# Kernel optimization log

Measured on AMD Instinct MI355X. Metric: run time of the kernel, lower is better.

## Reference

```python
import jax, jax.numpy as jnp
import numpy as np

NOPEN = 64
NNIN = 16
NUM_OUTPUT = 64
NLAYER = 4
H = 0.1
TF = 1.0
N_NODES = 50000
N_EDGES = 1600000


def setup_inputs() -> dict:
    key = jax.random.key(0)
    k1, k2, k3, k4, k5, k6 = jax.random.split(key, 6)
    xn = jax.random.normal(k1, (1, NNIN, N_NODES), dtype=jnp.float32)
    iInd = jax.random.randint(k2, (N_EDGES,), 0, N_NODES)
    jInd = jax.random.randint(k3, (N_EDGES,), 0, N_NODES)
    # learned parameters per original init
    K1Nopen = jax.random.normal(k4, (NOPEN, NNIN), dtype=jnp.float32) * 0.01
    KN1 = jnp.eye(NOPEN, dtype=jnp.float32) + jax.random.uniform(k5, (NOPEN, NOPEN), dtype=jnp.float32) * 0.001
    KNclose = jax.random.normal(k6, (NUM_OUTPUT, NOPEN), dtype=jnp.float32) * 0.01
    return {"xn": xn, "iInd": iInd, "jInd": jInd, "n_nodes": N_NODES,
            "K1Nopen": K1Nopen, "KN1": KN1, "KNclose": KNclose}


def _gcn_norm(I, J, n_nodes, dtype):
    # add self-loops, symmetric normalization deg^{-1/2}[row]*deg^{-1/2}[col]
    loops = jnp.arange(n_nodes, dtype=I.dtype)
    I2 = jnp.concatenate([I, loops])
    J2 = jnp.concatenate([J, loops])
    ew = jnp.ones(I2.shape[0], dtype=dtype)
    deg = jax.ops.segment_sum(ew, J2, num_segments=n_nodes)
    dinv = jnp.where(deg > 0, 1.0 / jnp.sqrt(deg), 0.0)
    w = dinv[I2] * dinv[J2]
    return I2, J2, w


def reference(xn, iInd, jInd, n_nodes, K1Nopen, KN1, KNclose):
    I, J, w = _gcn_norm(iInd, jInd, n_nodes, xn.dtype)  # [E+N]

    # OpenFlatLayer: 1x1 conv1d with K1Nopen + relu (openclose=True, norm=False)
    x = jax.nn.relu(jnp.einsum('oi,bin->bon', K1Nopen, xn))  # [1, nopen, N]

    dt = TF / NLAYER
    wb = w[None, None, :]
    for _ in range(NLAYER):
        # nodeGrad: edge features [1, nopen, E]
        g = wb * (x[:, :, I] - x[:, :, J])
        # singleLayer (openclose=False): conv(K), relu, conv(K.t())
        z = jax.nn.relu(jnp.einsum('oi,bie->boe', KN1, g))
        z = jnp.einsum('io,bie->boe', KN1, z)
        # edgeDiv: scatter-add w*z at I minus at J
        wz = jnp.moveaxis(wb * z, -1, 0)  # [E, 1, nopen]
        div = (jax.ops.segment_sum(wz, I, num_segments=n_nodes)
               - jax.ops.segment_sum(wz, J, num_segments=n_nodes))
        div = jnp.moveaxis(div, 0, -1)  # [1, nopen, N]
        # forward Euler: step layer returns -h*div, integrated with dt
        x = x - dt * H * div

    # CloseLayer: 1x1 conv1d, squeeze().t(), log_softmax over channels
    xc = jnp.einsum('oi,bin->bon', KNclose, x)[0].T  # [N, num_output]
    return jax.nn.log_softmax(xc, axis=1)
```

## Files before the change

kernel.cpp:

```cpp
#include <hip/hip_runtime.h>

#define NN 50000
#define NE 1600000
#define C 64
#define NIN 16
#define DTH 0.025f
#define ASC 16.0f
#define USC 64.0f
#define SDIV 16384.0f
#define SLOT 128

#define NB2 256
#define NPB 196
#define CAP 16384
#define ABLK 1024
#define EPB 1563
#define RND 2048
#define BINC 32
#define GSTR 16

typedef _Float16 f16x2 __attribute__((ext_vector_type(2)));
typedef float f32x2 __attribute__((ext_vector_type(2)));
union U32H2 { uint32_t u; f16x2 h; };

#define RL(x, l) __int_as_float(__builtin_amdgcn_readlane(__float_as_int(x), (l)))

__global__ void k_setup(const float* __restrict__ KN1, const float* __restrict__ KNc,
                        float* __restrict__ M2s, float* __restrict__ KMs,
                        int* __restrict__ gcur) {
    if (threadIdx.x < NB2) gcur[threadIdx.x * GSTR] = 0;
    for (int idx = threadIdx.x; idx < C * C; idx += blockDim.x) {
        int p = idx >> 6, o = idx & 63;
        float s1 = 0.f, s2 = 0.f;
        for (int i = 0; i < C; i++) {
            s1 = fmaf(KN1[o * C + i], KN1[p * C + i], s1);
            s2 = fmaf(KNc[o * C + i], KN1[p * C + i], s2);
        }
        M2s[idx] = s1;
        KMs[idx] = s2;
    }
}

static __device__ __forceinline__ void store_u8(uint32_t* __restrict__ u8, int n, int lane, float su) {
    float v1 = __shfl_down(su, 1, 64);
    float v2 = __shfl_down(su, 2, 64);
    float v3 = __shfl_down(su, 3, 64);
    if ((lane & 3) == 0) {
        int p0 = __builtin_amdgcn_cvt_pk_fp8_f32(su, v1, 0, false);
        int p1 = __builtin_amdgcn_cvt_pk_fp8_f32(v2, v3, p0, true);
        u8[n * 16 + (lane >> 2)] = (uint32_t)p1;
    }
}

__launch_bounds__(512)
__global__ void k_binA_open(const int* __restrict__ iInd, const int* __restrict__ jInd,
                            int* __restrict__ gcur, uint32_t* __restrict__ stg,
                            const float* __restrict__ xn, const float* __restrict__ K1,
                            const float* __restrict__ KN1, const float* __restrict__ KNc,
                            _Float16* __restrict__ u0, uint32_t* __restrict__ u8,
                            float* __restrict__ co) {
    __shared__ __align__(16) char smem[36864];
    __shared__ int bcnt[NB2];
    __shared__ int gbase[NB2];
    uint32_t (*bins)[BINC] = (uint32_t(*)[BINC])smem;
    int tid = threadIdx.x;
    int eBeg = blockIdx.x * EPB;
    int eEnd = eBeg + EPB; if (eEnd > NE) eEnd = NE;
    for (int rb = eBeg; rb < eEnd; rb += RND) {
        for (int b = tid; b < NB2; b += 512) bcnt[b] = 0;
        __syncthreads();
        int rEnd = rb + RND; if (rEnd > eEnd) rEnd = eEnd;
        for (int e = rb + tid; e < rEnd; e += 512) {
            int i = __builtin_nontemporal_load(&iInd[e]);
            int j = __builtin_nontemporal_load(&jInd[e]);
            {
                int b = (unsigned)i / NPB;
                uint32_t ent = ((unsigned)(i - b * NPB) << 17) | (unsigned)j;
                int pos = atomicAdd(&bcnt[b], 1);
                if (pos < BINC) bins[b][pos] = ent;
                else { int gp = atomicAdd(&gcur[b * GSTR], 1);
                       if (gp < CAP) stg[(size_t)b * CAP + gp] = ent; }
            }
            {
                int b = (unsigned)j / NPB;
                uint32_t ent = ((unsigned)(j - b * NPB) << 17) | 0x10000u | (unsigned)i;
                int pos = atomicAdd(&bcnt[b], 1);
                if (pos < BINC) bins[b][pos] = ent;
                else { int gp = atomicAdd(&gcur[b * GSTR], 1);
                       if (gp < CAP) stg[(size_t)b * CAP + gp] = ent; }
            }
        }
        __syncthreads();
        if (tid < NB2) {
            int c = bcnt[tid]; if (c > BINC) c = BINC;
            gbase[tid] = (c > 0) ? atomicAdd(&gcur[tid * GSTR], c) : 0;
        }
        __syncthreads();
        for (int idx = tid; idx < NB2 * BINC; idx += 512) {
            int b = idx >> 5, k = idx & (BINC - 1);
            int c = bcnt[b]; if (c > BINC) c = BINC;
            if (k < c) {
                int pos = gbase[b] + k;
                if (pos < CAP) stg[(size_t)b * CAP + pos] = bins[b][k];
            }
        }
        __syncthreads();
    }
    float* sK1 = (float*)smem;
    float* sU  = sK1 + NIN * C;
    float* sC  = sU + C * C;
    for (int idx = tid; idx < NIN * C; idx += 512) {
        int i = idx >> 6, o = idx & 63;
        sK1[idx] = K1[o * NIN + i];
    }
    for (int idx = tid; idx < C * C; idx += 512) {
        int o = idx >> 6, p = idx & 63;
        int sw = (o << 6) | (p ^ ((o & 7) << 2));
        sU[sw] = KN1[idx];
        sC[sw] = KNc[idx];
    }
    __syncthreads();
    int wv = tid >> 6, lane = tid & 63;
    int mb = lane << 6, lx = (lane & 7) << 2;
    for (int pr = blockIdx.x * 8 + wv; pr < NN / 2; pr += ABLK * 8) {
        int nA = pr * 2, nB = nA + 1;
        float xA = 0.f, xB = 0.f;
#pragma unroll
        for (int i = 0; i < NIN; i++) {
            float k1 = sK1[i * C + lane];
            xA = fmaf(k1, xn[i * NN + nA], xA);
            xB = fmaf(k1, xn[i * NN + nB], xB);
        }
        xA = fmaxf(xA, 0.f); xB = fmaxf(xB, 0.f);
        float uA0 = 0.f, uA1 = 0.f, uB0 = 0.f, uB1 = 0.f;
        float cA0 = 0.f, cA1 = 0.f, cB0 = 0.f, cB1 = 0.f;
#pragma unroll
        for (int p0 = 0; p0 < C; p0 += 4) {
            const float4 mu = *(const float4*)&sU[mb + (p0 ^ lx)];
            const float4 mc = *(const float4*)&sC[mb + (p0 ^ lx)];
            float a0 = RL(xA, p0 + 0), a1 = RL(xA, p0 + 1);
            float a2 = RL(xA, p0 + 2), a3 = RL(xA, p0 + 3);
            float b0 = RL(xB, p0 + 0), b1 = RL(xB, p0 + 1);
            float b2 = RL(xB, p0 + 2), b3 = RL(xB, p0 + 3);
            uA0 = fmaf(mu.x, a0, uA0); uA1 = fmaf(mu.y, a1, uA1);
            uA0 = fmaf(mu.z, a2, uA0); uA1 = fmaf(mu.w, a3, uA1);
            uB0 = fmaf(mu.x, b0, uB0); uB1 = fmaf(mu.y, b1, uB1);
            uB0 = fmaf(mu.z, b2, uB0); uB1 = fmaf(mu.w, b3, uB1);
            cA0 = fmaf(mc.x, a0, cA0); cA1 = fmaf(mc.y, a1, cA1);
            cA0 = fmaf(mc.z, a2, cA0); cA1 = fmaf(mc.w, a3, cA1);
            cB0 = fmaf(mc.x, b0, cB0); cB1 = fmaf(mc.y, b1, cB1);
            cB0 = fmaf(mc.z, b2, cB0); cB1 = fmaf(mc.w, b3, cB1);
        }
        float uA = uA0 + uA1, uB = uB0 + uB1;
        u0[(size_t)nA * C + lane] = (_Float16)uA;
        u0[(size_t)nB * C + lane] = (_Float16)uB;
        store_u8(u8, nA, lane, uA * USC);
        store_u8(u8, nB, lane, uB * USC);
        co[(size_t)nA * C + lane] = cA0 + cA1;
        co[(size_t)nB * C + lane] = cB0 + cB1;
    }
}

#define LADJ (NPB * SLOT)
__launch_bounds__(1024)
__global__ void k_binB(const int* __restrict__ gcur, const uint32_t* __restrict__ stg,
                       unsigned* __restrict__ pk, float* __restrict__ dinv,
                       uint32_t* __restrict__ adjp) {
    __shared__ unsigned lcnt[NPB];
    __shared__ uint32_t ladj[LADJ];
    int b = blockIdx.x, tid = threadIdx.x;
    if (tid < NPB) lcnt[tid] = 0;
    __syncthreads();
    int cnt = gcur[b * GSTR]; if (cnt > CAP) cnt = CAP;
    int n0 = b * NPB;
    for (int k = tid; k < cnt; k += 1024) {
        uint32_t ent = stg[(size_t)b * CAP + k];
        int tl = (int)(ent >> 17);
        unsigned sign = (ent >> 16) & 1u;
        unsigned other = ent & 0xFFFFu;
        unsigned ret = atomicAdd(&lcnt[tl], 1u + (sign << 16));
        unsigned slot = ret & 0xFFFFu;
        if (slot < SLOT) ladj[(tl << 7) + slot] = other | (sign << 31);
    }
    __syncthreads();
    if (tid < NPB) {
        int n = n0 + tid;
        if (n < NN) {
            unsigned v = lcnt[tid];
            unsigned c = v & 0xFFFFu; if (c > SLOT) c = SLOT;
            unsigned deg = (v >> 16) + 1u;
            pk[n] = (deg << 16) | c;
            dinv[n] = 1.0f / sqrtf((float)deg);
        }
    }
    int nval = NN - n0; if (nval > NPB) nval = NPB; if (nval < 0) nval = 0;
    int totv = (nval << 7) >> 2;
    uint4* gdst = (uint4*)(adjp + ((size_t)n0 << 7));
    const uint4* lsrc = (const uint4*)ladj;
    for (int v = tid; v < totv; v += 1024) gdst[v] = lsrc[v];
}

__global__ void k_weight(const unsigned* __restrict__ pk, const float* __restrict__ dinv,
                         uint32_t* __restrict__ adjp) {
    int idx = blockIdx.x * 256 + threadIdx.x;
    int n = idx >> 7, p = idx & (SLOT - 1);
    int cnt = (int)(pk[n] & 0xFFFFu); if (cnt > SLOT) cnt = SLOT;
    int pad = (cnt + 31) & ~31;
    if (p < cnt) {
        uint32_t e = adjp[idx];
        int other = (int)(e & 0xFFFFu);
        float a = ASC * dinv[n] * dinv[other];
        float w = 0.5f * a * a;
        if (e >> 31) w = -w;
        U32H2 t; t.u = (unsigned)other; t.h.y = (_Float16)w;
        adjp[idx] = t.u;
    } else if (p < pad) {
        adjp[idx] = 0u;
    }
}

#define ACCR(WW, QQ, A0, A1, A2, A3, U0, U1, U2, U3) {                        \
    U32H2 aw; aw.u = (WW);                                                    \
    float w_ = (float)aw.h.y;                                                 \
    f32x2 lo_ = __builtin_amdgcn_cvt_pk_f32_fp8((int)(QQ), false);            \
    f32x2 hi_ = __builtin_amdgcn_cvt_pk_f32_fp8((int)(QQ), true);             \
    float d0_ = (U0) - lo_.x, d1_ = (U1) - lo_.y;                             \
    float d2_ = (U2) - hi_.x, d3_ = (U3) - hi_.y;                             \
    A0 = fmaf(w_, __builtin_fabsf(d0_), fmaf(__builtin_fabsf(w_), d0_, A0));  \
    A1 = fmaf(w_, __builtin_fabsf(d1_), fmaf(__builtin_fabsf(w_), d1_, A1));  \
    A2 = fmaf(w_, __builtin_fabsf(d2_), fmaf(__builtin_fabsf(w_), d2_, A2));  \
    A3 = fmaf(w_, __builtin_fabsf(d3_), fmaf(__builtin_fabsf(w_), d3_, A3));  \
}

#define GATHER2_BODY(PKA, ADJP, U8R)                                          \
    uint32_t unqA = (U8R)[nA * 16 + li];                                      \
    uint32_t unqB = (U8R)[nB * 16 + li];                                      \
    f32x2 alo = __builtin_amdgcn_cvt_pk_f32_fp8((int)unqA, false);            \
    f32x2 ahi = __builtin_amdgcn_cvt_pk_f32_fp8((int)unqA, true);             \
    f32x2 blo = __builtin_amdgcn_cvt_pk_f32_fp8((int)unqB, false);            \
    f32x2 bhi = __builtin_amdgcn_cvt_pk_f32_fp8((int)unqB, true);             \
    float uA0 = alo.x, uA1 = alo.y, uA2 = ahi.x, uA3 = ahi.y;                 \
    float uB0 = blo.x, uB1 = blo.y, uB2 = bhi.x, uB3 = bhi.y;                 \
    uint2 pk2_ = *(const uint2*)&(PKA)[nA];                                   \
    int degA = (int)(pk2_.x & 0xFFFFu); if (degA > SLOT) degA = SLOT;         \
    int degB = (int)(pk2_.y & 0xFFFFu); if (degB > SLOT) degB = SLOT;         \
    int padA = (degA + 31) & ~31, padB = (degB + 31) & ~31;                   \
    int baseA = nA << 7, baseB = nB << 7;                                     \
    int maxPad = padA > padB ? padA : padB;                                   \
    float aA0 = 0.f, aA1 = 0.f, aA2 = 0.f, aA3 = 0.f;                         \
    float aB0 = 0.f, aB1 = 0.f, aB2 = 0.f, aB3 = 0.f;                         \
    for (int c0 = 0; c0 < maxPad; c0 += 32) {                                 \
        uint32_t wA[8], qA[8], wB[8], qB[8];                                  \
        bool dA = c0 < padA, dB = c0 < padB;                                  \
        if (dA) {                                                             \
            _Pragma("unroll")                                                 \
            for (int r = 0; r < 8; r++) wA[r] = (ADJP)[baseA + c0 + r * 4 + g]; \
        }                                                                     \
        if (dB) {                                                             \
            _Pragma("unroll")                                                 \
            for (int r = 0; r < 8; r++) wB[r] = (ADJP)[baseB + c0 + r * 4 + g]; \
        }                                                                     \
        if (dA) {                                                             \
            _Pragma("unroll")                                                 \
            for (int r = 0; r < 8; r++) qA[r] = (U8R)[(wA[r] & 0xFFFFu) * 16 + li]; \
        }                                                                     \
        if (dB) {                                                             \
            _Pragma("unroll")                                                 \
            for (int r = 0; r < 8; r++) qB[r] = (U8R)[(wB[r] & 0xFFFFu) * 16 + li]; \
        }                                                                     \
        if (dA) {                                                             \
            _Pragma("unroll")                                                 \
            for (int r = 0; r < 8; r++) ACCR(wA[r], qA[r], aA0, aA1, aA2, aA3, uA0, uA1, uA2, uA3) \
        }                                                                     \
        if (dB) {                                                             \
            _Pragma("unroll")                                                 \
            for (int r = 0; r < 8; r++) ACCR(wB[r], qB[r], aB0, aB1, aB2, aB3, uB0, uB1, uB2, uB3) \
        }                                                                     \
    }                                                                         \
    aA0 += __shfl_xor(aA0, 16, 64); aA0 += __shfl_xor(aA0, 32, 64);           \
    aA1 += __shfl_xor(aA1, 16, 64); aA1 += __shfl_xor(aA1, 32, 64);           \
    aA2 += __shfl_xor(aA2, 16, 64); aA2 += __shfl_xor(aA2, 32, 64);           \
    aA3 += __shfl_xor(aA3, 16, 64); aA3 += __shfl_xor(aA3, 32, 64);           \
    aB0 += __shfl_xor(aB0, 16, 64); aB0 += __shfl_xor(aB0, 32, 64);           \
    aB1 += __shfl_xor(aB1, 16, 64); aB1 += __shfl_xor(aB1, 32, 64);           \
    aB2 += __shfl_xor(aB2, 16, 64); aB2 += __shfl_xor(aB2, 32, 64);           \
    aB3 += __shfl_xor(aB3, 16, 64); aB3 += __shfl_xor(aB3, 32, 64);           \
    float rA0 = __shfl(aA0, lane >> 2, 64), rA1 = __shfl(aA1, lane >> 2, 64); \
    float rA2 = __shfl(aA2, lane >> 2, 64), rA3 = __shfl(aA3, lane >> 2, 64); \
    float rB0 = __shfl(aB0, lane >> 2, 64), rB1 = __shfl(aB1, lane >> 2, 64); \
    float rB2 = __shfl(aB2, lane >> 2, 64), rB3 = __shfl(aB3, lane >> 2, 64); \
    float sA_lane = (lane & 2) ? ((lane & 1) ? rA3 : rA2)                     \
                               : ((lane & 1) ? rA1 : rA0);                    \
    float sB_lane = (lane & 2) ? ((lane & 1) ? rB3 : rB2)                     \
                               : ((lane & 1) ? rB1 : rB0);

#define STAGE_MT(SMT, SRC) {                                                  \
    for (int idx = threadIdx.x; idx < C * C; idx += 256) {                    \
        int p_ = idx >> 6, c_ = idx & 63;                                     \
        (SMT)[(c_ << 6) | (p_ ^ ((c_ & 7) << 2))] = (SRC)[idx];               \
    }                                                                         \
}

#define MATVEC2(SMT, SAV, SBV, DUA, DUB) {                                    \
    float mA0_ = 0.f, mA1_ = 0.f, mB0_ = 0.f, mB1_ = 0.f;                     \
    int mb_ = (lane << 6), lx_ = (lane & 7) << 2;                             \
    _Pragma("unroll")                                                         \
    for (int p0 = 0; p0 < 64; p0 += 4) {                                      \
        const float4 mv = *(const float4*)&(SMT)[mb_ + (p0 ^ lx_)];           \
        mA0_ = fmaf(mv.x, RL(SAV, p0 + 0), mA0_);                             \
        mA1_ = fmaf(mv.y, RL(SAV, p0 + 1), mA1_);                             \
        mA0_ = fmaf(mv.z, RL(SAV, p0 + 2), mA0_);                             \
        mA1_ = fmaf(mv.w, RL(SAV, p0 + 3), mA1_);                             \
        mB0_ = fmaf(mv.x, RL(SBV, p0 + 0), mB0_);                             \
        mB1_ = fmaf(mv.y, RL(SBV, p0 + 1), mB1_);                             \
        mB0_ = fmaf(mv.z, RL(SBV, p0 + 2), mB0_);                             \
        mB1_ = fmaf(mv.w, RL(SBV, p0 + 3), mB1_);                             \
    }                                                                         \
    DUA = mA0_ + mA1_; DUB = mB0_ + mB1_;                                     \
}

__launch_bounds__(256, 8)
__global__ void k_gather_upd(const unsigned* __restrict__ pk, const uint32_t* __restrict__ adjp,
                             const uint32_t* __restrict__ u8r, const _Float16* __restrict__ ucur,
                             const float* __restrict__ M2s, float* __restrict__ sacc,
                             _Float16* __restrict__ unext, uint32_t* __restrict__ u8w, int beta) {
    __shared__ float sMt[C * C];
    STAGE_MT(sMt, M2s)
    __syncthreads();
    int wv = threadIdx.x >> 6, lane = threadIdx.x & 63;
    int g = lane >> 4, li = lane & 15;
    int nA = (blockIdx.x * 4 + wv) * 2;
    int nB = nA + 1;
    GATHER2_BODY(pk, adjp, u8r)
    float duA, duB;
    MATVEC2(sMt, sA_lane, sB_lane, duA, duB)
    float unewA = (float)ucur[(size_t)nA * C + lane] - (DTH / SDIV) * duA;
    float unewB = (float)ucur[(size_t)nB * C + lane] - (DTH / SDIV) * duB;
    unext[(size_t)nA * C + lane] = (_Float16)unewA;
    unext[(size_t)nB * C + lane] = (_Float16)unewB;
    store_u8(u8w, nA, lane, unewA * USC);
    store_u8(u8w, nB, lane, unewB * USC);
    size_t ixA = (size_t)nA * C + lane, ixB = (size_t)nB * C + lane;
    sacc[ixA] = beta ? (sacc[ixA] + sA_lane) : sA_lane;
    sacc[ixB] = beta ? (sacc[ixB] + sB_lane) : sB_lane;
}

__launch_bounds__(256, 8)
__global__ void k_gather_close(const unsigned* __restrict__ pk, const uint32_t* __restrict__ adjp,
                               const uint32_t* __restrict__ u8r, const float* __restrict__ KMs,
                               const float* __restrict__ sacc, const float* __restrict__ co,
                               float* __restrict__ out) {
    __shared__ float sKMt[C * C];
    STAGE_MT(sKMt, KMs)
    __syncthreads();
    int wv = threadIdx.x >> 6, lane = threadIdx.x & 63;
    int g = lane >> 4, li = lane & 15;
    int nA = (blockIdx.x * 4 + wv) * 2;
    int nB = nA + 1;
    GATHER2_BODY(pk, adjp, u8r)
    float stotA = sA_lane + sacc[(size_t)nA * C + lane];
    float stotB = sB_lane + sacc[(size_t)nB * C + lane];
    float dxA, dxB;
    MATVEC2(sKMt, stotA, stotB, dxA, dxB)
    float oA = co[(size_t)nA * C + lane] - (DTH / SDIV) * dxA;
    float oB = co[(size_t)nB * C + lane] - (DTH / SDIV) * dxB;
    float mA = oA, mB = oB;
#pragma unroll
    for (int off2 = 32; off2; off2 >>= 1) {
        mA = fmaxf(mA, __shfl_xor(mA, off2, 64));
        mB = fmaxf(mB, __shfl_xor(mB, off2, 64));
    }
    float sumA = expf(oA - mA), sumB = expf(oB - mB);
#pragma unroll
    for (int off2 = 32; off2; off2 >>= 1) {
        sumA += __shfl_xor(sumA, off2, 64);
        sumB += __shfl_xor(sumB, off2, 64);
    }
    out[(size_t)nA * C + lane] = oA - mA - logf(sumA);
    out[(size_t)nB * C + lane] = oB - mB - logf(sumB);
}

extern "C" void kernel_launch(void* const* d_in, const int* in_sizes, int n_in,
                              void* d_out, int out_size, void* d_ws, size_t ws_size,
                              hipStream_t stream) {
    (void)in_sizes; (void)n_in; (void)out_size; (void)ws_size;
    const float* xn   = (const float*)d_in[0];
    const int* iInd   = (const int*)d_in[1];
    const int* jInd   = (const int*)d_in[2];
    const float* K1   = (const float*)d_in[4];
    const float* KN1  = (const float*)d_in[5];
    const float* KNc  = (const float*)d_in[6];
    float* out = (float*)d_out;

    char* base = (char*)d_ws;
    size_t off = 0;
    auto alloc = [&](size_t bytes) { char* p = base + off; off = (off + bytes + 255) & ~(size_t)255; return p; };
    float* M2s  = (float*)alloc(C * C * 4);
    float* KMs  = (float*)alloc(C * C * 4);
    int* gcur   = (int*)alloc(NB2 * GSTR * 4);
    unsigned* pk = (unsigned*)alloc(NN * 4);
    float* dinv = (float*)alloc(NN * 4);
    float* co   = (float*)alloc((size_t)NN * C * 4);
    float* sacc = (float*)alloc((size_t)NN * C * 4);
    _Float16* ua = (_Float16*)alloc((size_t)NN * C * 2);
    _Float16* ub = (_Float16*)alloc((size_t)NN * C * 2);
    uint32_t* u8a = (uint32_t*)alloc((size_t)NN * 16 * 4);
    uint32_t* u8b = (uint32_t*)alloc((size_t)NN * 16 * 4);
    uint32_t* stg = (uint32_t*)alloc((size_t)NB2 * CAP * 4);
    uint32_t* adjp = (uint32_t*)alloc((size_t)NN * SLOT * 4);

    k_setup<<<1, 256, 0, stream>>>(KN1, KNc, M2s, KMs, gcur);
    k_binA_open<<<ABLK, 512, 0, stream>>>(iInd, jInd, gcur, stg, xn, K1, KN1, KNc, ua, u8a, co);
    k_binB<<<NB2, 1024, 0, stream>>>(gcur, stg, pk, dinv, adjp);
    k_weight<<<(NN * SLOT) / 256, 256, 0, stream>>>(pk, dinv, adjp);

    const int GB = NN / 8;
    k_gather_upd<<<GB, 256, 0, stream>>>(pk, adjp, u8a, ua, M2s, sacc, ub, u8b, 0);
    k_gather_upd<<<GB, 256, 0, stream>>>(pk, adjp, u8b, ub, M2s, sacc, ua, u8a, 1);
    k_gather_upd<<<GB, 256, 0, stream>>>(pk, adjp, u8a, ua, M2s, sacc, ub, u8b, 1);
    k_gather_close<<<GB, 256, 0, stream>>>(pk, adjp, u8b, KMs, sacc, co, out);
}
```

Baseline: 503.3 us.

## Compact padded adjacency into variable-length rows with global offset allocation

Replaces the fixed 128-slot-per-node adjacency with a compacted layout. Each row is padded only to a multiple of 32, and each bin block gets a contiguous region from a global atomic allocator. Bin construction now makes two passes over the staged entries (count, prefix-sum, place), and a per-node row offset array is read by the weight and gather kernels. The aim is to shrink the adjacency footprint and the bytes written, zeroed and copied, so gathers have better cache locality. The cost is an extra staging pass and a serial prefix scan in one thread per block.

```diff
diff --git a/kernel.cpp b/kernel.cpp
--- a/kernel.cpp
+++ b/kernel.cpp
@@ -18,6 +18,7 @@
 #define RND 2048
 #define BINC 32
 #define GSTR 16
+#define LIMG 20480
 
 typedef _Float16 f16x2 __attribute__((ext_vector_type(2)));
 typedef float f32x2 __attribute__((ext_vector_type(2)));
@@ -27,8 +28,9 @@
 
 __global__ void k_setup(const float* __restrict__ KN1, const float* __restrict__ KNc,
                         float* __restrict__ M2s, float* __restrict__ KMs,
-                        int* __restrict__ gcur) {
+                        int* __restrict__ gcur, unsigned* __restrict__ galloc) {
     if (threadIdx.x < NB2) gcur[threadIdx.x * GSTR] = 0;
+    if (threadIdx.x == 0) galloc[0] = 0;
     for (int idx = threadIdx.x; idx < C * C; idx += blockDim.x) {
         int p = idx >> 6, o = idx & 63;
         float s1 = 0.f, s2 = 0.f;
@@ -161,15 +163,18 @@
     }
 }
 
-#define LADJ (NPB * SLOT)
 __launch_bounds__(1024)
 __global__ void k_binB(const int* __restrict__ gcur, const uint32_t* __restrict__ stg,
                        unsigned* __restrict__ pk, float* __restrict__ dinv,
-                       uint32_t* __restrict__ adjp) {
+                       unsigned* __restrict__ rowoff, uint32_t* __restrict__ adjp,
+                       unsigned* __restrict__ galloc) {
     __shared__ unsigned lcnt[NPB];
-    __shared__ uint32_t ladj[LADJ];
+    __shared__ unsigned soff[NPB];
+    __shared__ unsigned place[NPB];
+    __shared__ uint32_t ladj[LIMG];
+    __shared__ unsigned sb[2];
     int b = blockIdx.x, tid = threadIdx.x;
-    if (tid < NPB) lcnt[tid] = 0;
+    if (tid < NPB) { lcnt[tid] = 0; place[tid] = 0; }
     __syncthreads();
     int cnt = gcur[b * GSTR]; if (cnt > CAP) cnt = CAP;
     int n0 = b * NPB;
@@ -177,10 +182,37 @@
         uint32_t ent = stg[(size_t)b * CAP + k];
         int tl = (int)(ent >> 17);
         unsigned sign = (ent >> 16) & 1u;
+        atomicAdd(&lcnt[tl], 1u + (sign << 16));
+    }
+    __syncthreads();
+    if (tid == 0) {
+        unsigned run = 0;
+        for (int t = 0; t < NPB; t++) {
+            unsigned c = lcnt[t] & 0xFFFFu; if (c > SLOT) c = SLOT;
+            soff[t] = run;
+            run += (c + 31u) & ~31u;
+        }
+        sb[1] = run;
+        sb[0] = atomicAdd(galloc, run);
+    }
+    __syncthreads();
+    unsigned bbase = sb[0], total = sb[1];
+    unsigned totl = total < LIMG ? total : LIMG;
+    for (unsigned k = tid; k < totl; k += 1024) ladj[k] = 0u;
+    for (unsigned k = LIMG + tid; k < total; k += 1024) adjp[bbase + k] = 0u;
+    __syncthreads();
+    for (int k = tid; k < cnt; k += 1024) {
+        uint32_t ent = stg[(size_t)b * CAP + k];
+        int tl = (int)(ent >> 17);
+        unsigned sign = (ent >> 16) & 1u;
         unsigned other = ent & 0xFFFFu;
-        unsigned ret = atomicAdd(&lcnt[tl], 1u + (sign << 16));
-        unsigned slot = ret & 0xFFFFu;
-        if (slot < SLOT) ladj[(tl << 7) + slot] = other | (sign << 31);
+        unsigned slot = atomicAdd(&place[tl], 1u);
+        if (slot < SLOT) {
+            unsigned pos = soff[tl] + slot;
+            uint32_t val = other | (sign << 31);
+            if (pos < LIMG) ladj[pos] = val;
+            else adjp[bbase + pos] = val;
+        }
     }
     __syncthreads();
     if (tid < NPB) {
@@ -191,31 +223,29 @@
             unsigned deg = (v >> 16) + 1u;
             pk[n] = (deg << 16) | c;
             dinv[n] = 1.0f / sqrtf((float)deg);
-        }
-    }
-    int nval = NN - n0; if (nval > NPB) nval = NPB; if (nval < 0) nval = 0;
-    int totv = (nval << 7) >> 2;
-    uint4* gdst = (uint4*)(adjp + ((size_t)n0 << 7));
+            rowoff[n] = bbase + soff[tid];
+        }
+    }
+    uint4* gdst = (uint4*)(adjp + bbase);
     const uint4* lsrc = (const uint4*)ladj;
-    for (int v = tid; v < totv; v += 1024) gdst[v] = lsrc[v];
-}
-
-__global__ void k_weight(const unsigned* __restrict__ pk, const float* __restrict__ dinv,
-                         uint32_t* __restrict__ adjp) {
-    int idx = blockIdx.x * 256 + threadIdx.x;
-    int n = idx >> 7, p = idx & (SLOT - 1);
+    for (unsigned v = tid; v < (totl >> 2); v += 1024) gdst[v] = lsrc[v];
+}
+
+__launch_bounds__(256)
+__global__ void k_weight(const unsigned* __restrict__ pk, const unsigned* __restrict__ rowoff,
+                         const float* __restrict__ dinv, uint32_t* __restrict__ adjp) {
+    int n = blockIdx.x * 2 + (threadIdx.x >> 7);
+    int p = threadIdx.x & (SLOT - 1);
     int cnt = (int)(pk[n] & 0xFFFFu); if (cnt > SLOT) cnt = SLOT;
-    int pad = (cnt + 31) & ~31;
     if (p < cnt) {
-        uint32_t e = adjp[idx];
+        unsigned base = rowoff[n];
+        uint32_t e = adjp[base + p];
         int other = (int)(e & 0xFFFFu);
         float a = ASC * dinv[n] * dinv[other];
         float w = 0.5f * a * a;
         if (e >> 31) w = -w;
         U32H2 t; t.u = (unsigned)other; t.h.y = (_Float16)w;
-        adjp[idx] = t.u;
-    } else if (p < pad) {
-        adjp[idx] = 0u;
+        adjp[base + p] = t.u;
     }
 }
 
@@ -232,7 +262,7 @@
     A3 = fmaf(w_, __builtin_fabsf(d3_), fmaf(__builtin_fabsf(w_), d3_, A3));  \
 }
 
-#define GATHER2_BODY(PKA, ADJP, U8R)                                          \
+#define GATHER2_BODY(PKA, ROFF, ADJP, U8R)                                    \
     uint32_t unqA = (U8R)[nA * 16 + li];                                      \
     uint32_t unqB = (U8R)[nB * 16 + li];                                      \
     f32x2 alo = __builtin_amdgcn_cvt_pk_f32_fp8((int)unqA, false);            \
@@ -242,10 +272,11 @@
     float uA0 = alo.x, uA1 = alo.y, uA2 = ahi.x, uA3 = ahi.y;                 \
     float uB0 = blo.x, uB1 = blo.y, uB2 = bhi.x, uB3 = bhi.y;                 \
     uint2 pk2_ = *(const uint2*)&(PKA)[nA];                                   \
+    uint2 ro2_ = *(const uint2*)&(ROFF)[nA];                                  \
     int degA = (int)(pk2_.x & 0xFFFFu); if (degA > SLOT) degA = SLOT;         \
     int degB = (int)(pk2_.y & 0xFFFFu); if (degB > SLOT) degB = SLOT;         \
     int padA = (degA + 31) & ~31, padB = (degB + 31) & ~31;                   \
-    int baseA = nA << 7, baseB = nB << 7;                                     \
+    int baseA = (int)ro2_.x, baseB = (int)ro2_.y;                             \
     int maxPad = padA > padB ? padA : padB;                                   \
     float aA0 = 0.f, aA1 = 0.f, aA2 = 0.f, aA3 = 0.f;                         \
     float aB0 = 0.f, aB1 = 0.f, aB2 = 0.f, aB3 = 0.f;                         \
@@ -320,7 +351,8 @@
 }
 
 __launch_bounds__(256, 8)
-__global__ void k_gather_upd(const unsigned* __restrict__ pk, const uint32_t* __restrict__ adjp,
+__global__ void k_gather_upd(const unsigned* __restrict__ pk, const unsigned* __restrict__ rowoff,
+                             const uint32_t* __restrict__ adjp,
                              const uint32_t* __restrict__ u8r, const _Float16* __restrict__ ucur,
                              const float* __restrict__ M2s, float* __restrict__ sacc,
                              _Float16* __restrict__ unext, uint32_t* __restrict__ u8w, int beta) {
@@ -331,7 +363,7 @@
     int g = lane >> 4, li = lane & 15;
     int nA = (blockIdx.x * 4 + wv) * 2;
     int nB = nA + 1;
-    GATHER2_BODY(pk, adjp, u8r)
+    GATHER2_BODY(pk, rowoff, adjp, u8r)
     float duA, duB;
     MATVEC2(sMt, sA_lane, sB_lane, duA, duB)
     float unewA = (float)ucur[(size_t)nA * C + lane] - (DTH / SDIV) * duA;
@@ -346,7 +378,8 @@
 }
 
 __launch_bounds__(256, 8)
-__global__ void k_gather_close(const unsigned* __restrict__ pk, const uint32_t* __restrict__ adjp,
+__global__ void k_gather_close(const unsigned* __restrict__ pk, const unsigned* __restrict__ rowoff,
+                               const uint32_t* __restrict__ adjp,
                                const uint32_t* __restrict__ u8r, const float* __restrict__ KMs,
                                const float* __restrict__ sacc, const float* __restrict__ co,
                                float* __restrict__ out) {
@@ -357,7 +390,7 @@
     int g = lane >> 4, li = lane & 15;
     int nA = (blockIdx.x * 4 + wv) * 2;
     int nB = nA + 1;
-    GATHER2_BODY(pk, adjp, u8r)
+    GATHER2_BODY(pk, rowoff, adjp, u8r)
     float stotA = sA_lane + sacc[(size_t)nA * C + lane];
     float stotB = sB_lane + sacc[(size_t)nB * C + lane];
     float dxA, dxB;
@@ -398,7 +431,9 @@
     float* M2s  = (float*)alloc(C * C * 4);
     float* KMs  = (float*)alloc(C * C * 4);
     int* gcur   = (int*)alloc(NB2 * GSTR * 4);
+    unsigned* galloc = (unsigned*)alloc(256);
     unsigned* pk = (unsigned*)alloc(NN * 4);
+    unsigned* rowoff = (unsigned*)alloc((NN + 2) * 4);
     float* dinv = (float*)alloc(NN * 4);
     float* co   = (float*)alloc((size_t)NN * C * 4);
     float* sacc = (float*)alloc((size_t)NN * C * 4);
@@ -409,14 +444,14 @@
     uint32_t* stg = (uint32_t*)alloc((size_t)NB2 * CAP * 4);
     uint32_t* adjp = (uint32_t*)alloc((size_t)NN * SLOT * 4);
 
-    k_setup<<<1, 256, 0, stream>>>(KN1, KNc, M2s, KMs, gcur);
+    k_setup<<<1, 256, 0, stream>>>(KN1, KNc, M2s, KMs, gcur, galloc);
     k_binA_open<<<ABLK, 512, 0, stream>>>(iInd, jInd, gcur, stg, xn, K1, KN1, KNc, ua, u8a, co);
-    k_binB<<<NB2, 1024, 0, stream>>>(gcur, stg, pk, dinv, adjp);
-    k_weight<<<(NN * SLOT) / 256, 256, 0, stream>>>(pk, dinv, adjp);
+    k_binB<<<NB2, 1024, 0, stream>>>(gcur, stg, pk, dinv, rowoff, adjp, galloc);
+    k_weight<<<NN / 2, 256, 0, stream>>>(pk, rowoff, dinv, adjp);
 
     const int GB = NN / 8;
-    k_gather_upd<<<GB, 256, 0, stream>>>(pk, adjp, u8a, ua, M2s, sacc, ub, u8b, 0);
-    k_gather_upd<<<GB, 256, 0, stream>>>(pk, adjp, u8b, ub, M2s, sacc, ua, u8a, 1);
-    k_gather_upd<<<GB, 256, 0, stream>>>(pk, adjp, u8a, ua, M2s, sacc, ub, u8b, 1);
-    k_gather_close<<<GB, 256, 0, stream>>>(pk, adjp, u8b, KMs, sacc, co, out);
-}
+    k_gather_upd<<<GB, 256, 0, stream>>>(pk, rowoff, adjp, u8a, ua, M2s, sacc, ub, u8b, 0);
+    k_gather_upd<<<GB, 256, 0, stream>>>(pk, rowoff, adjp, u8b, ub, M2s, sacc, ua, u8a, 1);
+    k_gather_upd<<<GB, 256, 0, stream>>>(pk, rowoff, adjp, u8a, ua, M2s, sacc, ub, u8b, 1);
+    k_gather_close<<<GB, 256, 0, stream>>>(pk, rowoff, adjp, u8b, KMs, sacc, co, out);
+}
```

New measurement: 510.3 us. Within noise of the previous version (+1.4%).

## Fuse edge weight computation into first gather pass and drop k_weight kernel

Applied to the files above, without the earlier changes.

Removes the separate k_weight kernel that rewrote the whole padded adjacency with fp16 edge weights. The first gather layer now loads dinv for each neighbour, computes the signed normalized weight inline, uses it directly, and writes it back into the adjacency for later layers. k_binB now zero-fills the local adjacency so padding entries are already zero. This saves one kernel launch and a full pass over the adjacency buffer, at the cost of an extra dinv gather and predicated stores in the first layer.

```diff
diff --git a/kernel.cpp b/kernel.cpp
--- a/kernel.cpp
+++ b/kernel.cpp
@@ -170,6 +170,7 @@
     __shared__ uint32_t ladj[LADJ];
     int b = blockIdx.x, tid = threadIdx.x;
     if (tid < NPB) lcnt[tid] = 0;
+    for (int k = tid; k < LADJ; k += 1024) ladj[k] = 0u;
     __syncthreads();
     int cnt = gcur[b * GSTR]; if (cnt > CAP) cnt = CAP;
     int n0 = b * NPB;
@@ -200,39 +201,18 @@
     for (int v = tid; v < totv; v += 1024) gdst[v] = lsrc[v];
 }
 
-__global__ void k_weight(const unsigned* __restrict__ pk, const float* __restrict__ dinv,
-                         uint32_t* __restrict__ adjp) {
-    int idx = blockIdx.x * 256 + threadIdx.x;
-    int n = idx >> 7, p = idx & (SLOT - 1);
-    int cnt = (int)(pk[n] & 0xFFFFu); if (cnt > SLOT) cnt = SLOT;
-    int pad = (cnt + 31) & ~31;
-    if (p < cnt) {
-        uint32_t e = adjp[idx];
-        int other = (int)(e & 0xFFFFu);
-        float a = ASC * dinv[n] * dinv[other];
-        float w = 0.5f * a * a;
-        if (e >> 31) w = -w;
-        U32H2 t; t.u = (unsigned)other; t.h.y = (_Float16)w;
-        adjp[idx] = t.u;
-    } else if (p < pad) {
-        adjp[idx] = 0u;
-    }
-}
-
-#define ACCR(WW, QQ, A0, A1, A2, A3, U0, U1, U2, U3) {                        \
-    U32H2 aw; aw.u = (WW);                                                    \
-    float w_ = (float)aw.h.y;                                                 \
+#define ACCR_W(W_, QQ, A0, A1, A2, A3, U0, U1, U2, U3) {                      \
     f32x2 lo_ = __builtin_amdgcn_cvt_pk_f32_fp8((int)(QQ), false);            \
     f32x2 hi_ = __builtin_amdgcn_cvt_pk_f32_fp8((int)(QQ), true);             \
     float d0_ = (U0) - lo_.x, d1_ = (U1) - lo_.y;                             \
     float d2_ = (U2) - hi_.x, d3_ = (U3) - hi_.y;                             \
-    A0 = fmaf(w_, __builtin_fabsf(d0_), fmaf(__builtin_fabsf(w_), d0_, A0));  \
-    A1 = fmaf(w_, __builtin_fabsf(d1_), fmaf(__builtin_fabsf(w_), d1_, A1));  \
-    A2 = fmaf(w_, __builtin_fabsf(d2_), fmaf(__builtin_fabsf(w_), d2_, A2));  \
-    A3 = fmaf(w_, __builtin_fabsf(d3_), fmaf(__builtin_fabsf(w_), d3_, A3));  \
-}
-
-#define GATHER2_BODY(PKA, ADJP, U8R)                                          \
+    A0 = fmaf((W_), __builtin_fabsf(d0_), fmaf(__builtin_fabsf(W_), d0_, A0)); \
+    A1 = fmaf((W_), __builtin_fabsf(d1_), fmaf(__builtin_fabsf(W_), d1_, A1)); \
+    A2 = fmaf((W_), __builtin_fabsf(d2_), fmaf(__builtin_fabsf(W_), d2_, A2)); \
+    A3 = fmaf((W_), __builtin_fabsf(d3_), fmaf(__builtin_fabsf(W_), d3_, A3)); \
+}
+
+#define GATHER2_BODY(PKA, ADJP, U8R, FIRSTF, DINV)                            \
     uint32_t unqA = (U8R)[nA * 16 + li];                                      \
     uint32_t unqB = (U8R)[nB * 16 + li];                                      \
     f32x2 alo = __builtin_amdgcn_cvt_pk_f32_fp8((int)unqA, false);            \
@@ -247,10 +227,13 @@
     int padA = (degA + 31) & ~31, padB = (degB + 31) & ~31;                   \
     int baseA = nA << 7, baseB = nB << 7;                                     \
     int maxPad = padA > padB ? padA : padB;                                   \
+    float dnA = 0.f, dnB = 0.f;                                               \
+    if (FIRSTF) { dnA = ASC * (DINV)[nA]; dnB = ASC * (DINV)[nB]; }           \
     float aA0 = 0.f, aA1 = 0.f, aA2 = 0.f, aA3 = 0.f;                         \
     float aB0 = 0.f, aB1 = 0.f, aB2 = 0.f, aB3 = 0.f;                         \
     for (int c0 = 0; c0 < maxPad; c0 += 32) {                                 \
         uint32_t wA[8], qA[8], wB[8], qB[8];                                  \
+        float vA[8], vB[8];                                                   \
         bool dA = c0 < padA, dB = c0 < padB;                                  \
         if (dA) {                                                             \
             _Pragma("unroll")                                                 \
@@ -260,6 +243,16 @@
             _Pragma("unroll")                                                 \
             for (int r = 0; r < 8; r++) wB[r] = (ADJP)[baseB + c0 + r * 4 + g]; \
         }                                                                     \
+        if (FIRSTF) {                                                         \
+            if (dA) {                                                         \
+                _Pragma("unroll")                                             \
+                for (int r = 0; r < 8; r++) vA[r] = (DINV)[wA[r] & 0xFFFFu];  \
+            }                                                                 \
+            if (dB) {                                                         \
+                _Pragma("unroll")                                             \
+                for (int r = 0; r < 8; r++) vB[r] = (DINV)[wB[r] & 0xFFFFu];  \
+            }                                                                 \
+        }                                                                     \
         if (dA) {                                                             \
             _Pragma("unroll")                                                 \
             for (int r = 0; r < 8; r++) qA[r] = (U8R)[(wA[r] & 0xFFFFu) * 16 + li]; \
@@ -270,11 +263,39 @@
         }                                                                     \
         if (dA) {                                                             \
             _Pragma("unroll")                                                 \
-            for (int r = 0; r < 8; r++) ACCR(wA[r], qA[r], aA0, aA1, aA2, aA3, uA0, uA1, uA2, uA3) \
+            for (int r = 0; r < 8; r++) {                                     \
+                float wgt_;                                                   \
+                if (FIRSTF) {                                                 \
+                    float a_ = dnA * vA[r];                                   \
+                    float wf_ = 0.5f * a_ * a_;                               \
+                    wf_ = __int_as_float(__float_as_int(wf_) ^ (int)(wA[r] & 0x80000000u)); \
+                    if ((c0 + r * 4 + g) >= degA) wf_ = 0.f;                  \
+                    U32H2 t_; t_.u = wA[r] & 0xFFFFu; t_.h.y = (_Float16)wf_; \
+                    wgt_ = (float)t_.h.y;     \
+                    if (li == 2 * r) ((uint32_t*)(ADJP))[baseA + c0 + r * 4 + g] = t_.u; \
+                } else {                                                      \
+                    U32H2 aw_; aw_.u = wA[r]; wgt_ = (float)aw_.h.y;          \
+                }                                                             \
+                ACCR_W(wgt_, qA[r], aA0, aA1, aA2, aA3, uA0, uA1, uA2, uA3)   \
+            }                                                                 \
         }                                                                     \
         if (dB) {                                                             \
             _Pragma("unroll")                                                 \
-            for (int r = 0; r < 8; r++) ACCR(wB[r], qB[r], aB0, aB1, aB2, aB3, uB0, uB1, uB2, uB3) \
+            for (int r = 0; r < 8; r++) {                                     \
+                float wgt_;                                                   \
+                if (FIRSTF) {                                                 \
+                    float a_ = dnB * vB[r];                                   \
+                    float wf_ = 0.5f * a_ * a_;                               \
+                    wf_ = __int_as_float(__float_as_int(wf_) ^ (int)(wB[r] & 0x80000000u)); \
+                    if ((c0 + r * 4 + g) >= degB) wf_ = 0.f;                  \
+                    U32H2 t_; t_.u = wB[r] & 0xFFFFu; t_.h.y = (_Float16)wf_; \
+                    wgt_ = (float)t_.h.y;                                     \
+                    if (li == 2 * r) ((uint32_t*)(ADJP))[baseB + c0 + r * 4 + g] = t_.u; \
+                } else {                                                      \
+                    U32H2 aw_; aw_.u = wB[r]; wgt_ = (float)aw_.h.y;          \
+                }                                                             \
+                ACCR_W(wgt_, qB[r], aB0, aB1, aB2, aB3, uB0, uB1, uB2, uB3)   \
+            }                                                                 \
         }                                                                     \
     }                                                                         \
     aA0 += __shfl_xor(aA0, 16, 64); aA0 += __shfl_xor(aA0, 32, 64);           \
@@ -319,11 +340,13 @@
     DUA = mA0_ + mA1_; DUB = mB0_ + mB1_;                                     \
 }
 
+template<int FIRST>
 __launch_bounds__(256, 8)
-__global__ void k_gather_upd(const unsigned* __restrict__ pk, const uint32_t* __restrict__ adjp,
+__global__ void k_gather_upd(const unsigned* __restrict__ pk, uint32_t* __restrict__ adjp,
                              const uint32_t* __restrict__ u8r, const _Float16* __restrict__ ucur,
                              const float* __restrict__ M2s, float* __restrict__ sacc,
-                             _Float16* __restrict__ unext, uint32_t* __restrict__ u8w, int beta) {
+                             _Float16* __restrict__ unext, uint32_t* __restrict__ u8w, int beta,
+                             const float* __restrict__ dinv) {
     __shared__ float sMt[C * C];
     STAGE_MT(sMt, M2s)
     __syncthreads();
@@ -331,7 +354,7 @@
     int g = lane >> 4, li = lane & 15;
     int nA = (blockIdx.x * 4 + wv) * 2;
     int nB = nA + 1;
-    GATHER2_BODY(pk, adjp, u8r)
+    GATHER2_BODY(pk, adjp, u8r, FIRST, dinv)
     float duA, duB;
     MATVEC2(sMt, sA_lane, sB_lane, duA, duB)
     float unewA = (float)ucur[(size_t)nA * C + lane] - (DTH / SDIV) * duA;
@@ -346,7 +369,7 @@
 }
 
 __launch_bounds__(256, 8)
-__global__ void k_gather_close(const unsigned* __restrict__ pk, const uint32_t* __restrict__ adjp,
+__global__ void k_gather_close(const unsigned* __restrict__ pk, uint32_t* __restrict__ adjp,
                                const uint32_t* __restrict__ u8r, const float* __restrict__ KMs,
                                const float* __restrict__ sacc, const float* __restrict__ co,
                                float* __restrict__ out) {
@@ -357,7 +380,7 @@
     int g = lane >> 4, li = lane & 15;
     int nA = (blockIdx.x * 4 + wv) * 2;
     int nB = nA + 1;
-    GATHER2_BODY(pk, adjp, u8r)
+    GATHER2_BODY(pk, adjp, u8r, 0, co)
     float stotA = sA_lane + sacc[(size_t)nA * C + lane];
     float stotB = sB_lane + sacc[(size_t)nB * C + lane];
     float dxA, dxB;
@@ -412,11 +435,10 @@
     k_setup<<<1, 256, 0, stream>>>(KN1, KNc, M2s, KMs, gcur);
     k_binA_open<<<ABLK, 512, 0, stream>>>(iInd, jInd, gcur, stg, xn, K1, KN1, KNc, ua, u8a, co);
     k_binB<<<NB2, 1024, 0, stream>>>(gcur, stg, pk, dinv, adjp);
-    k_weight<<<(NN * SLOT) / 256, 256, 0, stream>>>(pk, dinv, adjp);
 
     const int GB = NN / 8;
-    k_gather_upd<<<GB, 256, 0, stream>>>(pk, adjp, u8a, ua, M2s, sacc, ub, u8b, 0);
-    k_gather_upd<<<GB, 256, 0, stream>>>(pk, adjp, u8b, ub, M2s, sacc, ua, u8a, 1);
-    k_gather_upd<<<GB, 256, 0, stream>>>(pk, adjp, u8a, ua, M2s, sacc, ub, u8b, 1);
+    k_gather_upd<1><<<GB, 256, 0, stream>>>(pk, adjp, u8a, ua, M2s, sacc, ub, u8b, 0, dinv);
+    k_gather_upd<0><<<GB, 256, 0, stream>>>(pk, adjp, u8b, ub, M2s, sacc, ua, u8a, 1, dinv);
+    k_gather_upd<0><<<GB, 256, 0, stream>>>(pk, adjp, u8a, ua, M2s, sacc, ub, u8b, 1, dinv);
     k_gather_close<<<GB, 256, 0, stream>>>(pk, adjp, u8b, KMs, sacc, co, out);
 }
```

Result: slower. 651.3 us (+29.4%).
